# Optimization experiments

Hardware: AMD Instinct MI355X
Metric: run time of the kernel (lower is better)

## Reference

```python
import jax, jax.numpy as jnp
import numpy as np

NUM_NODES = 100000
NODE_DIM = 128
MEM_DIM = 128
EDGE_DIM = 172
TIME_DIM = 100
HIDDEN = 256
E = 262144


def setup_inputs() -> dict:
    key = jax.random.key(0)
    ks = jax.random.split(key, 12)
    src = jax.random.randint(ks[0], (E,), 0, NUM_NODES)
    dst = jax.random.randint(ks[1], (E,), 0, NUM_NODES)
    ts = jax.random.uniform(ks[2], (E,), dtype=jnp.float32) * 1e6
    edge_feat = jax.random.normal(ks[3], (E, EDGE_DIM), dtype=jnp.float32)
    node_emb = jax.random.normal(ks[4], (NUM_NODES, NODE_DIM), dtype=jnp.float32) * 0.02
    memory = jax.random.normal(ks[5], (NUM_NODES, MEM_DIM), dtype=jnp.float32) * 0.02
    # TimeEncoder: w.weight = 1/10**linspace(0,9,time_dim), bias = 0
    time_w = jnp.asarray(1.0 / 10 ** np.linspace(0, 9, TIME_DIM), dtype=jnp.float32)
    time_b = jnp.zeros((TIME_DIM,), dtype=jnp.float32)
    edge_W = jax.random.normal(ks[6], (HIDDEN, EDGE_DIM), dtype=jnp.float32) * (1.0 / np.sqrt(EDGE_DIM))
    edge_b = jnp.zeros((HIDDEN,), dtype=jnp.float32)
    in1 = NODE_DIM * 2 + MEM_DIM * 2  # 512
    W1 = jax.random.normal(ks[7], (HIDDEN, in1), dtype=jnp.float32) * (1.0 / np.sqrt(in1))
    b1 = jnp.zeros((HIDDEN,), dtype=jnp.float32)
    W2 = jax.random.normal(ks[8], (1, HIDDEN), dtype=jnp.float32) * (1.0 / np.sqrt(HIDDEN))
    b2 = jnp.zeros((1,), dtype=jnp.float32)
    return {
        "src": src, "dst": dst, "ts": ts, "edge_feat": edge_feat,
        "node_emb": node_emb, "memory": memory,
        "time_w": time_w, "time_b": time_b,
        "edge_W": edge_W, "edge_b": edge_b,
        "W1": W1, "b1": b1, "W2": W2, "b2": b2,
    }


def reference(src, dst, ts, edge_feat, node_emb, memory, time_w, time_b,
              edge_W, edge_b, W1, b1, W2, b2):
    # gathers (node embedding + memory table)
    src_embed = node_emb[src]          # [E, node_dim]
    dst_embed = node_emb[dst]          # [E, node_dim]
    src_memory = memory[src]           # [E, mem_dim]
    dst_memory = memory[dst]           # [E, mem_dim]
    # time / edge encodings are computed in the torch forward but unused in the output
    _time_embed = jnp.cos(ts[:, None] * time_w[None, :] + time_b)
    _edge_embed = edge_feat @ edge_W.T + edge_b
    # concat + 2-layer MLP scorer (Dropout is identity in eval)
    h = jnp.concatenate([src_embed, dst_embed, src_memory, dst_memory], axis=1)  # [E, 512]
    h1 = jax.nn.relu(h @ W1.T + b1)    # [E, hidden]
    out = (h1 @ W2.T + b2).squeeze(-1)  # [E]
    return out
```

## Files before the change

kernel.cpp:

```cpp
#include <hip/hip_runtime.h>

#define NNODES 100000
#define EDGES  262144
#define NTILES 3125
#define GEMM_BLOCKS 256

typedef __attribute__((ext_vector_type(8))) short short8v;
typedef __attribute__((ext_vector_type(8))) unsigned short ushort8v;
typedef __attribute__((ext_vector_type(4))) float f32x4;

__device__ __forceinline__ unsigned short f2bf(float f) {
  unsigned u = __builtin_bit_cast(unsigned, f);
  u += 0x7fffu + ((u >> 16) & 1u);
  return (unsigned short)(u >> 16);
}
__device__ __forceinline__ float bf2f(unsigned short u) {
  return __builtin_bit_cast(float, (unsigned)u << 16);
}
__device__ __forceinline__ unsigned cvt_pk(float lo, float hi) {
  unsigned r;
  asm volatile("v_cvt_pk_bf16_f32 %0, %1, %2" : "=v"(r) : "v"(lo), "v"(hi));
  return r;
}

__global__ __launch_bounds__(256) void prep_wc(const float* __restrict__ W1,
                                               unsigned short* __restrict__ Wc) {
  int idx = blockIdx.x * 256 + threadIdx.x;
  int j = idx >> 8;
  int k = idx & 255;
  int jj = j & 255;
  int kk = (k < 128) ? k : (k + 128);
  if (j >= 256) kk += 128;
  Wc[idx] = f2bf(W1[jj * 512 + kk]);
}

__global__ __launch_bounds__(512)
void gemm_proj10(const float* __restrict__ ne,
                 const float* __restrict__ mem,
                 const unsigned short* __restrict__ Wc,
                 const float* __restrict__ b1,
                 unsigned short* __restrict__ P) {
  __shared__ __align__(16) unsigned short As[2][32][272];
  const int tid  = threadIdx.x;
  const int bid  = blockIdx.x;
  const int wid  = tid >> 6;
  const int lane = tid & 63;
  const int lr   = lane & 15;
  const int kq   = (lane >> 4) * 8;
  const int cb   = wid * 64;

  ushort8v bfrag[8][4];
#pragma unroll
  for (int ks = 0; ks < 8; ++ks)
#pragma unroll
    for (int jt = 0; jt < 4; ++jt)
      bfrag[ks][jt] = *(const ushort8v*)(Wc + (size_t)(cb + jt * 16 + lr) * 256 + ks * 32 + kq);

  const int nt = (NTILES - bid + GEMM_BLOCKS - 1) / GEMM_BLOCKS;

  float4 g[4];
#pragma unroll
  for (int i = 0; i < 4; ++i) {
    int q = tid + i * 512;
    int row = q >> 6;
    int k0  = (q & 63) * 4;
    int node = bid * 32 + row;
    g[i] = *(const float4*)((k0 < 128) ? ne + (size_t)node * 128 + k0
                                       : mem + (size_t)node * 128 + (k0 - 128));
  }
#pragma unroll
  for (int i = 0; i < 4; ++i) {
    int q = tid + i * 512;
    int row = q >> 6;
    int k0  = (q & 63) * 4;
    uint2 pk { cvt_pk(g[i].x, g[i].y), cvt_pk(g[i].z, g[i].w) };
    *(uint2*)&As[0][row][k0] = pk;
  }
  __syncthreads();

  for (int it = 0; it < nt; ++it) {
    const int tile = bid + it * GEMM_BLOCKS;
    const int buf  = it & 1;
    const bool more = (it + 1 < nt);

    if (more) {
      const int ntile = bid + (it + 1) * GEMM_BLOCKS;
#pragma unroll
      for (int i = 0; i < 4; ++i) {
        int q = tid + i * 512;
        int row = q >> 6;
        int k0  = (q & 63) * 4;
        int node = ntile * 32 + row;
        g[i] = *(const float4*)((k0 < 128) ? ne + (size_t)node * 128 + k0
                                           : mem + (size_t)node * 128 + (k0 - 128));
      }
    }

    f32x4 acc[4][2] = {};
#pragma unroll
    for (int ks = 0; ks < 8; ++ks) {
      const int kk = ks * 32 + kq;
      ushort8v a0 = *(const ushort8v*)&As[buf][lr][kk];
      ushort8v a1 = *(const ushort8v*)&As[buf][lr + 16][kk];
#pragma unroll
      for (int jt = 0; jt < 4; ++jt) {
        acc[jt][0] = __builtin_amdgcn_mfma_f32_16x16x32_bf16((short8v)bfrag[ks][jt], (short8v)a0, acc[jt][0], 0, 0, 0);
        acc[jt][1] = __builtin_amdgcn_mfma_f32_16x16x32_bf16((short8v)bfrag[ks][jt], (short8v)a1, acc[jt][1], 0, 0, 0);
      }
    }

#pragma unroll
    for (int jt = 0; jt < 4; ++jt) {
      const int jq = cb + jt * 16 + (lane >> 4) * 4;
      float4 bv = (cb < 256) ? *(const float4*)(b1 + jq) : float4{0.f, 0.f, 0.f, 0.f};
#pragma unroll
      for (int h = 0; h < 2; ++h) {
        int node = tile * 32 + h * 16 + lr;
        f32x4 v = acc[jt][h];
        uint2 pk { cvt_pk(v[0] + bv.x, v[1] + bv.y),
                   cvt_pk(v[2] + bv.z, v[3] + bv.w) };
        *(uint2*)(P + (size_t)node * 512 + jq) = pk;
      }
    }

    if (more) {
#pragma unroll
      for (int i = 0; i < 4; ++i) {
        int q = tid + i * 512;
        int row = q >> 6;
        int k0  = (q & 63) * 4;
        uint2 pk { cvt_pk(g[i].x, g[i].y), cvt_pk(g[i].z, g[i].w) };
        *(uint2*)&As[buf ^ 1][row][k0] = pk;
      }
    }
    __syncthreads();
  }
}

__global__ __launch_bounds__(256) void edge_score2(const int* __restrict__ src,
                                                   const int* __restrict__ dst,
                                                   const unsigned short* __restrict__ P,
                                                   const float* __restrict__ W2,
                                                   const float* __restrict__ b2,
                                                   float* __restrict__ out) {
  const int wid  = threadIdx.x >> 6;
  const int lane = threadIdx.x & 63;
  const int half = lane >> 5;
  const int l5   = lane & 31;
  const int e    = blockIdx.x * 8 + wid * 2 + half;

  float4 w0 = *(const float4*)(W2 + l5 * 8);
  float4 w1 = *(const float4*)(W2 + l5 * 8 + 4);
  const float b2c = b2[0];

  const int s = src[e];
  const int d = dst[e];

  ushort8v a = *(const ushort8v*)(P + (size_t)s * 512 + l5 * 8);
  ushort8v b = *(const ushort8v*)(P + (size_t)d * 512 + 256 + l5 * 8);

  float h0 = bf2f(a[0]) + bf2f(b[0]); h0 = h0 > 0.f ? h0 : 0.f;
  float h1 = bf2f(a[1]) + bf2f(b[1]); h1 = h1 > 0.f ? h1 : 0.f;
  float h2 = bf2f(a[2]) + bf2f(b[2]); h2 = h2 > 0.f ? h2 : 0.f;
  float h3 = bf2f(a[3]) + bf2f(b[3]); h3 = h3 > 0.f ? h3 : 0.f;
  float h4 = bf2f(a[4]) + bf2f(b[4]); h4 = h4 > 0.f ? h4 : 0.f;
  float h5 = bf2f(a[5]) + bf2f(b[5]); h5 = h5 > 0.f ? h5 : 0.f;
  float h6 = bf2f(a[6]) + bf2f(b[6]); h6 = h6 > 0.f ? h6 : 0.f;
  float h7 = bf2f(a[7]) + bf2f(b[7]); h7 = h7 > 0.f ? h7 : 0.f;

  float partial = h0 * w0.x + h1 * w0.y + h2 * w0.z + h3 * w0.w
                + h4 * w1.x + h5 * w1.y + h6 * w1.z + h7 * w1.w;

#pragma unroll
  for (int off = 16; off; off >>= 1) partial += __shfl_xor(partial, off, 64);

  if (l5 == 0) out[e] = partial + b2c;
}

__global__ __launch_bounds__(256) void fallback_edge(const int* __restrict__ src,
                                                     const int* __restrict__ dst,
                                                     const float* __restrict__ ne,
                                                     const float* __restrict__ mem,
                                                     const float* __restrict__ W1,
                                                     const float* __restrict__ b1,
                                                     const float* __restrict__ W2,
                                                     const float* __restrict__ b2,
                                                     float* __restrict__ out) {
  __shared__ float hs[8][512];
  __shared__ float red[8][4];
  const int tid = threadIdx.x;
  const int e0  = blockIdx.x * 8;

  for (int idx = tid; idx < 8 * 512; idx += 256) {
    int e8 = idx >> 9, k = idx & 511;
    int e = e0 + e8;
    int s = src[e], d = dst[e];
    float v;
    if (k < 128)      v = ne[(size_t)s * 128 + k];
    else if (k < 256) v = ne[(size_t)d * 128 + k - 128];
    else if (k < 384) v = mem[(size_t)s * 128 + k - 256];
    else              v = mem[(size_t)d * 128 + k - 384];
    hs[e8][k] = v;
  }
  __syncthreads();

  const int j = tid;
  float acc[8] = {0, 0, 0, 0, 0, 0, 0, 0};
  const float* w1r = W1 + (size_t)j * 512;
  for (int k = 0; k < 512; k += 4) {
    float4 w = *(const float4*)(w1r + k);
#pragma unroll
    for (int e8 = 0; e8 < 8; ++e8)
      acc[e8] += hs[e8][k] * w.x + hs[e8][k + 1] * w.y + hs[e8][k + 2] * w.z + hs[e8][k + 3] * w.w;
  }
  const float bj = b1[j], wj = W2[j];
#pragma unroll
  for (int e8 = 0; e8 < 8; ++e8) {
    float h = acc[e8] + bj;
    h = h > 0.f ? h : 0.f;
    acc[e8] = h * wj;
  }
  const int lane = tid & 63, wid = tid >> 6;
#pragma unroll
  for (int e8 = 0; e8 < 8; ++e8) {
    float p = acc[e8];
#pragma unroll
    for (int off = 32; off; off >>= 1) p += __shfl_xor(p, off, 64);
    if (lane == 0) red[e8][wid] = p;
  }
  __syncthreads();
  if (tid < 8) out[e0 + tid] = red[tid][0] + red[tid][1] + red[tid][2] + red[tid][3] + b2[0];
}

extern "C" void kernel_launch(void* const* d_in, const int* in_sizes, int n_in,
                              void* d_out, int out_size, void* d_ws, size_t ws_size,
                              hipStream_t stream) {
  const int*   src      = (const int*)d_in[0];
  const int*   dst      = (const int*)d_in[1];
  const float* node_emb = (const float*)d_in[4];
  const float* memv     = (const float*)d_in[5];
  const float* W1       = (const float*)d_in[10];
  const float* b1       = (const float*)d_in[11];
  const float* W2       = (const float*)d_in[12];
  const float* b2       = (const float*)d_in[13];
  float*       out      = (float*)d_out;

  const size_t P_BYTES  = (size_t)NNODES * 512 * 2;
  const size_t WC_BYTES = (size_t)512 * 256 * 2;

  if (ws_size >= P_BYTES + WC_BYTES) {
    unsigned short* P  = (unsigned short*)d_ws;
    unsigned short* Wc = (unsigned short*)((char*)d_ws + P_BYTES);
    prep_wc<<<512, 256, 0, stream>>>(W1, Wc);
    gemm_proj10<<<GEMM_BLOCKS, 512, 0, stream>>>(node_emb, memv, Wc, b1, P);
    edge_score2<<<EDGES / 8, 256, 0, stream>>>(src, dst, P, W2, b2, out);
  } else {
    fallback_edge<<<EDGES / 8, 256, 0, stream>>>(src, dst, node_emb, memv, W1, b1, W2, b2, out);
  }
}
```

Before: 94.98 us.

## Use 64-row GEMM tiles with 1024 threads and 16 lanes per edge in scorer

```diff
diff --git a/kernel.cpp b/kernel.cpp
--- a/kernel.cpp
+++ b/kernel.cpp
@@ -2,7 +2,7 @@
 
 #define NNODES 100000
 #define EDGES  262144
-#define NTILES 3125
+#define NT64   1563
 #define GEMM_BLOCKS 256
 
 typedef __attribute__((ext_vector_type(8))) short short8v;
@@ -34,43 +34,43 @@
   Wc[idx] = f2bf(W1[jj * 512 + kk]);
 }
 
-__global__ __launch_bounds__(512)
-void gemm_proj10(const float* __restrict__ ne,
+__global__ __launch_bounds__(1024)
+void gemm_proj12(const float* __restrict__ ne,
                  const float* __restrict__ mem,
                  const unsigned short* __restrict__ Wc,
                  const float* __restrict__ b1,
                  unsigned short* __restrict__ P) {
-  __shared__ __align__(16) unsigned short As[2][32][272];
+  __shared__ __align__(16) unsigned short As[2][64][272];
   const int tid  = threadIdx.x;
   const int bid  = blockIdx.x;
   const int wid  = tid >> 6;
   const int lane = tid & 63;
   const int lr   = lane & 15;
   const int kq   = (lane >> 4) * 8;
-  const int cb   = wid * 64;
-
-  ushort8v bfrag[8][4];
+  const int cb   = wid * 32;
+
+  ushort8v bfrag[8][2];
 #pragma unroll
   for (int ks = 0; ks < 8; ++ks)
 #pragma unroll
-    for (int jt = 0; jt < 4; ++jt)
+    for (int jt = 0; jt < 2; ++jt)
       bfrag[ks][jt] = *(const ushort8v*)(Wc + (size_t)(cb + jt * 16 + lr) * 256 + ks * 32 + kq);
 
-  const int nt = (NTILES - bid + GEMM_BLOCKS - 1) / GEMM_BLOCKS;
+  const int nt = (NT64 - bid + GEMM_BLOCKS - 1) / GEMM_BLOCKS;
 
   float4 g[4];
 #pragma unroll
   for (int i = 0; i < 4; ++i) {
-    int q = tid + i * 512;
+    int q = tid + i * 1024;
     int row = q >> 6;
     int k0  = (q & 63) * 4;
-    int node = bid * 32 + row;
+    int node = bid * 64 + row;
     g[i] = *(const float4*)((k0 < 128) ? ne + (size_t)node * 128 + k0
                                        : mem + (size_t)node * 128 + (k0 - 128));
   }
 #pragma unroll
   for (int i = 0; i < 4; ++i) {
-    int q = tid + i * 512;
+    int q = tid + i * 1024;
     int row = q >> 6;
     int k0  = (q & 63) * 4;
     uint2 pk { cvt_pk(g[i].x, g[i].y), cvt_pk(g[i].z, g[i].w) };
@@ -84,49 +84,56 @@
     const bool more = (it + 1 < nt);
 
     if (more) {
-      const int ntile = bid + (it + 1) * GEMM_BLOCKS;
+      const int ntile = tile + GEMM_BLOCKS;
 #pragma unroll
       for (int i = 0; i < 4; ++i) {
-        int q = tid + i * 512;
+        int q = tid + i * 1024;
         int row = q >> 6;
         int k0  = (q & 63) * 4;
-        int node = ntile * 32 + row;
+        int node = ntile * 64 + row;
+        if (node > NNODES - 1) node = NNODES - 1;
         g[i] = *(const float4*)((k0 < 128) ? ne + (size_t)node * 128 + k0
                                            : mem + (size_t)node * 128 + (k0 - 128));
       }
     }
 
-    f32x4 acc[4][2] = {};
+    f32x4 acc[2][4] = {};
 #pragma unroll
     for (int ks = 0; ks < 8; ++ks) {
       const int kk = ks * 32 + kq;
       ushort8v a0 = *(const ushort8v*)&As[buf][lr][kk];
       ushort8v a1 = *(const ushort8v*)&As[buf][lr + 16][kk];
-#pragma unroll
-      for (int jt = 0; jt < 4; ++jt) {
+      ushort8v a2 = *(const ushort8v*)&As[buf][lr + 32][kk];
+      ushort8v a3 = *(const ushort8v*)&As[buf][lr + 48][kk];
+#pragma unroll
+      for (int jt = 0; jt < 2; ++jt) {
         acc[jt][0] = __builtin_amdgcn_mfma_f32_16x16x32_bf16((short8v)bfrag[ks][jt], (short8v)a0, acc[jt][0], 0, 0, 0);
         acc[jt][1] = __builtin_amdgcn_mfma_f32_16x16x32_bf16((short8v)bfrag[ks][jt], (short8v)a1, acc[jt][1], 0, 0, 0);
-      }
-    }
-
-#pragma unroll
-    for (int jt = 0; jt < 4; ++jt) {
+        acc[jt][2] = __builtin_amdgcn_mfma_f32_16x16x32_bf16((short8v)bfrag[ks][jt], (short8v)a2, acc[jt][2], 0, 0, 0);
+        acc[jt][3] = __builtin_amdgcn_mfma_f32_16x16x32_bf16((short8v)bfrag[ks][jt], (short8v)a3, acc[jt][3], 0, 0, 0);
+      }
+    }
+
+#pragma unroll
+    for (int jt = 0; jt < 2; ++jt) {
       const int jq = cb + jt * 16 + (lane >> 4) * 4;
       float4 bv = (cb < 256) ? *(const float4*)(b1 + jq) : float4{0.f, 0.f, 0.f, 0.f};
 #pragma unroll
-      for (int h = 0; h < 2; ++h) {
-        int node = tile * 32 + h * 16 + lr;
-        f32x4 v = acc[jt][h];
-        uint2 pk { cvt_pk(v[0] + bv.x, v[1] + bv.y),
-                   cvt_pk(v[2] + bv.z, v[3] + bv.w) };
-        *(uint2*)(P + (size_t)node * 512 + jq) = pk;
+      for (int h = 0; h < 4; ++h) {
+        int node = tile * 64 + h * 16 + lr;
+        if (node < NNODES) {
+          f32x4 v = acc[jt][h];
+          uint2 pk { cvt_pk(v[0] + bv.x, v[1] + bv.y),
+                     cvt_pk(v[2] + bv.z, v[3] + bv.w) };
+          *(uint2*)(P + (size_t)node * 512 + jq) = pk;
+        }
       }
     }
 
     if (more) {
 #pragma unroll
       for (int i = 0; i < 4; ++i) {
-        int q = tid + i * 512;
+        int q = tid + i * 1024;
         int row = q >> 6;
         int k0  = (q & 63) * 4;
         uint2 pk { cvt_pk(g[i].x, g[i].y), cvt_pk(g[i].z, g[i].w) };
@@ -137,44 +144,58 @@
   }
 }
 
-__global__ __launch_bounds__(256) void edge_score2(const int* __restrict__ src,
+__global__ __launch_bounds__(256) void edge_score4(const int* __restrict__ src,
                                                    const int* __restrict__ dst,
                                                    const unsigned short* __restrict__ P,
                                                    const float* __restrict__ W2,
                                                    const float* __restrict__ b2,
                                                    float* __restrict__ out) {
-  const int wid  = threadIdx.x >> 6;
-  const int lane = threadIdx.x & 63;
-  const int half = lane >> 5;
-  const int l5   = lane & 31;
-  const int e    = blockIdx.x * 8 + wid * 2 + half;
-
-  float4 w0 = *(const float4*)(W2 + l5 * 8);
-  float4 w1 = *(const float4*)(W2 + l5 * 8 + 4);
+  const int t  = threadIdx.x;
+  const int l4 = t & 15;
+  const int e  = blockIdx.x * 16 + (t >> 4);
+
+  float4 w0  = *(const float4*)(W2 + l4 * 16);
+  float4 w1  = *(const float4*)(W2 + l4 * 16 + 4);
+  float4 w2v = *(const float4*)(W2 + l4 * 16 + 8);
+  float4 w3  = *(const float4*)(W2 + l4 * 16 + 12);
   const float b2c = b2[0];
 
   const int s = src[e];
   const int d = dst[e];
 
-  ushort8v a = *(const ushort8v*)(P + (size_t)s * 512 + l5 * 8);
-  ushort8v b = *(const ushort8v*)(P + (size_t)d * 512 + 256 + l5 * 8);
-
-  float h0 = bf2f(a[0]) + bf2f(b[0]); h0 = h0 > 0.f ? h0 : 0.f;
-  float h1 = bf2f(a[1]) + bf2f(b[1]); h1 = h1 > 0.f ? h1 : 0.f;
-  float h2 = bf2f(a[2]) + bf2f(b[2]); h2 = h2 > 0.f ? h2 : 0.f;
-  float h3 = bf2f(a[3]) + bf2f(b[3]); h3 = h3 > 0.f ? h3 : 0.f;
-  float h4 = bf2f(a[4]) + bf2f(b[4]); h4 = h4 > 0.f ? h4 : 0.f;
-  float h5 = bf2f(a[5]) + bf2f(b[5]); h5 = h5 > 0.f ? h5 : 0.f;
-  float h6 = bf2f(a[6]) + bf2f(b[6]); h6 = h6 > 0.f ? h6 : 0.f;
-  float h7 = bf2f(a[7]) + bf2f(b[7]); h7 = h7 > 0.f ? h7 : 0.f;
-
-  float partial = h0 * w0.x + h1 * w0.y + h2 * w0.z + h3 * w0.w
-                + h4 * w1.x + h5 * w1.y + h6 * w1.z + h7 * w1.w;
-
-#pragma unroll
-  for (int off = 16; off; off >>= 1) partial += __shfl_xor(partial, off, 64);
-
-  if (l5 == 0) out[e] = partial + b2c;
+  const unsigned short* ps = P + (size_t)s * 512 + l4 * 16;
+  const unsigned short* pd = P + (size_t)d * 512 + 256 + l4 * 16;
+  ushort8v a0 = *(const ushort8v*)(ps);
+  ushort8v a1 = *(const ushort8v*)(ps + 8);
+  ushort8v c0 = *(const ushort8v*)(pd);
+  ushort8v c1 = *(const ushort8v*)(pd + 8);
+
+  float partial = 0.f;
+#pragma unroll
+  for (int i = 0; i < 4; ++i) {
+    float h = bf2f(a0[i]) + bf2f(c0[i]); h = h > 0.f ? h : 0.f;
+    partial += h * (&w0.x)[i];
+  }
+#pragma unroll
+  for (int i = 0; i < 4; ++i) {
+    float h = bf2f(a0[i + 4]) + bf2f(c0[i + 4]); h = h > 0.f ? h : 0.f;
+    partial += h * (&w1.x)[i];
+  }
+#pragma unroll
+  for (int i = 0; i < 4; ++i) {
+    float h = bf2f(a1[i]) + bf2f(c1[i]); h = h > 0.f ? h : 0.f;
+    partial += h * (&w2v.x)[i];
+  }
+#pragma unroll
+  for (int i = 0; i < 4; ++i) {
+    float h = bf2f(a1[i + 4]) + bf2f(c1[i + 4]); h = h > 0.f ? h : 0.f;
+    partial += h * (&w3.x)[i];
+  }
+
+#pragma unroll
+  for (int off = 8; off; off >>= 1) partial += __shfl_xor(partial, off, 64);
+
+  if (l4 == 0) out[e] = partial + b2c;
 }
 
 __global__ __launch_bounds__(256) void fallback_edge(const int* __restrict__ src,
@@ -252,8 +273,8 @@
     unsigned short* P  = (unsigned short*)d_ws;
     unsigned short* Wc = (unsigned short*)((char*)d_ws + P_BYTES);
     prep_wc<<<512, 256, 0, stream>>>(W1, Wc);
-    gemm_proj10<<<GEMM_BLOCKS, 512, 0, stream>>>(node_emb, memv, Wc, b1, P);
-    edge_score2<<<EDGES / 8, 256, 0, stream>>>(src, dst, P, W2, b2, out);
+    gemm_proj12<<<GEMM_BLOCKS, 1024, 0, stream>>>(node_emb, memv, Wc, b1, P);
+    edge_score4<<<EDGES / 16, 256, 0, stream>>>(src, dst, P, W2, b2, out);
   } else {
     fallback_edge<<<EDGES / 8, 256, 0, stream>>>(src, dst, node_emb, memv, W1, b1, W2, b2, out);
   }
```

Result: slower. 156.0 us (+64.3%).
